# Optimization experiments

Measured on AMD Instinct MI355X. Metric: run time of the kernel, lower is better.

The kernel has to match this reference:

```python
import jax, jax.numpy as jnp
import numpy as np

EPS_DIST = 1e-8   # matches 1.0/(dist + 1e-08) in the torch module
NEG_SLOPE = 0.2   # deep_gcns act_layer leakyrelu default
BN_EPS = 1e-5


def setup_inputs() -> dict:
    key = jax.random.key(0)
    ks = jax.random.split(key, 6)
    B, N, M = 8, 2048, 8192
    C, C_skip = 512, 256
    C_in = C + C_skip          # 768
    H1, H2 = 512, 256          # up_conv_nn = [768, 512, 256]
    pos = jax.random.normal(ks[0], (B, N, 3), dtype=jnp.float32)
    pos_skip = jax.random.normal(ks[1], (B, M, 3), dtype=jnp.float32)
    x = jax.random.normal(ks[2], (B, C, N), dtype=jnp.float32)
    x_skip = jax.random.normal(ks[3], (B, C_skip, M), dtype=jnp.float32)
    W1 = jax.random.normal(ks[4], (H1, C_in), dtype=jnp.float32) * (1.0 / np.sqrt(C_in))
    W2 = jax.random.normal(ks[5], (H2, H1), dtype=jnp.float32) * (1.0 / np.sqrt(H1))
    return {
        "pos": pos, "pos_skip": pos_skip, "x": x, "x_skip": x_skip,
        "W1": W1, "gamma1": jnp.ones((H1,), jnp.float32), "beta1": jnp.zeros((H1,), jnp.float32),
        "W2": W2, "gamma2": jnp.ones((H2,), jnp.float32), "beta2": jnp.zeros((H2,), jnp.float32),
    }


def _three_nn(query, ref):
    # query: [B, M, 3], ref: [B, N, 3] -> dist [B, M, 3], idx [B, M, 3]
    q2 = jnp.sum(query * query, axis=-1)                 # [B, M]
    r2 = jnp.sum(ref * ref, axis=-1)                     # [B, N]
    d2 = q2[:, :, None] + r2[:, None, :] - 2.0 * jnp.einsum('bmd,bnd->bmn', query, ref)
    neg_d2, idx = jax.lax.top_k(-d2, 3)                  # 3 smallest squared dists
    dist = jnp.sqrt(jnp.maximum(-neg_d2, 0.0))           # tp.three_nn returns L2 distance
    return dist, idx


def _three_interpolate(x, idx, weight):
    # x: [B, C, N], idx: [B, M, 3], weight: [B, M, 3] -> [B, C, M]
    xT = jnp.transpose(x, (0, 2, 1))                     # [B, N, C]
    gathered = jax.vmap(lambda f, i: f[i])(xT, idx)      # [B, M, 3, C]
    return jnp.einsum('bmkc,bmk->bcm', gathered, weight)


def _bn_act(h, gamma, beta):
    # training-mode BatchNorm1d over (batch, points) + LeakyReLU
    mean = jnp.mean(h, axis=(0, 2), keepdims=True)
    var = jnp.mean((h - mean) ** 2, axis=(0, 2), keepdims=True)
    h = (h - mean) * jax.lax.rsqrt(var + BN_EPS)
    h = h * gamma[None, :, None] + beta[None, :, None]
    return jnp.where(h >= 0, h, NEG_SLOPE * h)


def reference(pos, pos_skip, x, x_skip, W1, gamma1, beta1, W2, gamma2, beta2):
    # 3-NN of each fine point (pos_skip) among coarse points (pos)
    dist, idx = _three_nn(pos_skip, pos)
    dist_recip = 1.0 / (dist + EPS_DIST)
    norm = jnp.sum(dist_recip, axis=2, keepdims=True)
    weight = dist_recip / norm                           # [B, M, 3]
    interpolated = _three_interpolate(x, idx, weight)    # [B, C, M]
    feats = jnp.concatenate([interpolated, x_skip], axis=1)  # [B, C+C_skip, M]
    # MLP: Conv1d(k=1, bias=False) -> BN -> LeakyReLU, twice
    h = jnp.einsum('oi,bim->bom', W1, feats)
    h = _bn_act(h, gamma1, beta1)
    h = jnp.einsum('oi,bim->bom', W2, h)
    h = _bn_act(h, gamma2, beta2)
    return h  # [B, 256, M]
```

## Files before the change

### kernel.cpp

```cpp
#include <hip/hip_runtime.h>
#include <stdint.h>

#define B_    8
#define N_    2048
#define M_    8192
#define C_    512
#define CSK   256
#define CIN   768
#define H1C   512
#define H2C   256
#define NCOL  65536
typedef unsigned short u16;
typedef __attribute__((ext_vector_type(8))) short  s16x8;
typedef __attribute__((ext_vector_type(4))) float  f32x4;

__device__ inline u16 f2bf(float f) {
    unsigned u = __float_as_uint(f);
    unsigned r = (u + 0x7fffu + ((u >> 16) & 1u)) >> 16;
    return (u16)r;
}
__device__ inline float bflo(unsigned u) { return __uint_as_float(u << 16); }
__device__ inline float bfhi(unsigned u) { return __uint_as_float(u & 0xffff0000u); }

__global__ __launch_bounds__(256) void cvt_bf16_k(const float* __restrict__ in,
                                                  u16* __restrict__ out, int n4) {
    const int i = blockIdx.x * 256 + threadIdx.x;
    if (i >= n4) return;
    const float4 v = *(const float4*)(in + (size_t)i * 4);
    u16 o[4] = {f2bf(v.x), f2bf(v.y), f2bf(v.z), f2bf(v.w)};
    *(uint2*)(out + (size_t)i * 4) = *(uint2*)o;
}

__device__ inline void ins3(float d, int n,
                            float& d0, int& i0, float& d1, int& i1,
                            float& d2, int& i2) {
    const bool lt0 = d < d0, lt1 = d < d1, lt2 = d < d2;
    const float nd2 = lt1 ? d1 : (lt2 ? d : d2);
    const int   ni2 = lt1 ? i1 : (lt2 ? n : i2);
    const float nd1 = lt0 ? d0 : (lt1 ? d : d1);
    const int   ni1 = lt0 ? i0 : (lt1 ? n : i1);
    const float nd0 = lt0 ? d : d0;
    const int   ni0 = lt0 ? n : i0;
    d0 = nd0; d1 = nd1; d2 = nd2; i0 = ni0; i1 = ni1; i2 = ni2;
}

__global__ __launch_bounds__(256) void knn_kernel(const float* __restrict__ pos,
                                                  const float* __restrict__ pos_skip,
                                                  int* __restrict__ idx_out,
                                                  float* __restrict__ w_out) {
    __shared__ float rpx[N_], rpy[N_], rpz[N_], rr2[N_];
    const int b = blockIdx.y;
    const int tid = threadIdx.x;
    for (int t = tid; t < N_ * 3; t += 256) {
        const float v = pos[(size_t)b * N_ * 3 + t];
        const int n = t / 3, k = t - n * 3;
        if (k == 0) rpx[n] = v; else if (k == 1) rpy[n] = v; else rpz[n] = v;
    }
    __syncthreads();
    for (int n = tid; n < N_; n += 256)
        rr2[n] = rpx[n] * rpx[n] + rpy[n] * rpy[n] + rpz[n] * rpz[n];
    __syncthreads();

    const int q = tid >> 3;
    const int part = tid & 7;
    const int m = blockIdx.x * 32 + q;
    const size_t qoff = ((size_t)b * M_ + m) * 3;
    const float qx = pos_skip[qoff], qy = pos_skip[qoff + 1], qz = pos_skip[qoff + 2];
    const float q2x = -2.0f * qx, q2y = -2.0f * qy, q2z = -2.0f * qz;
    const float qq = qx * qx + qy * qy + qz * qz;

    float d0 = 1e30f, d1 = 1e30f, d2 = 1e30f;
    int i0 = 0, i1 = 0, i2 = 0;
#pragma unroll 4
    for (int i = 0; i < 64; ++i) {
        const int n = part * 4 + i * 32;
        const float4 xx = *(const float4*)&rpx[n];
        const float4 yy = *(const float4*)&rpy[n];
        const float4 zz = *(const float4*)&rpz[n];
        const float4 ww = *(const float4*)&rr2[n];
        const float s0 = fmaf(xx.x, q2x, fmaf(yy.x, q2y, fmaf(zz.x, q2z, ww.x)));
        const float s1 = fmaf(xx.y, q2x, fmaf(yy.y, q2y, fmaf(zz.y, q2z, ww.y)));
        const float s2 = fmaf(xx.z, q2x, fmaf(yy.z, q2y, fmaf(zz.z, q2z, ww.z)));
        const float s3 = fmaf(xx.w, q2x, fmaf(yy.w, q2y, fmaf(zz.w, q2z, ww.w)));
        ins3(s0, n + 0, d0, i0, d1, i1, d2, i2);
        ins3(s1, n + 1, d0, i0, d1, i1, d2, i2);
        ins3(s2, n + 2, d0, i0, d1, i1, d2, i2);
        ins3(s3, n + 3, d0, i0, d1, i1, d2, i2);
    }

#pragma unroll
    for (int xm = 1; xm <= 4; xm <<= 1) {
        const float od0 = __shfl_xor(d0, xm), od1 = __shfl_xor(d1, xm), od2 = __shfl_xor(d2, xm);
        const int   oi0 = __shfl_xor(i0, xm), oi1 = __shfl_xor(i1, xm), oi2 = __shfl_xor(i2, xm);
        ins3(od0, oi0, d0, i0, d1, i1, d2, i2);
        ins3(od1, oi1, d0, i0, d1, i1, d2, i2);
        ins3(od2, oi2, d0, i0, d1, i1, d2, i2);
    }

    if (part == 0) {
        const float dd0 = fmaxf(d0 + qq, 0.f);
        const float dd1 = fmaxf(d1 + qq, 0.f);
        const float dd2 = fmaxf(d2 + qq, 0.f);
        const float r0 = 1.0f / (sqrtf(dd0) + 1e-8f);
        const float r1 = 1.0f / (sqrtf(dd1) + 1e-8f);
        const float r2 = 1.0f / (sqrtf(dd2) + 1e-8f);
        const float inv = 1.0f / (r0 + r1 + r2);
        const size_t o = ((size_t)b * M_ + m) * 3;
        idx_out[o] = i0; idx_out[o + 1] = i1; idx_out[o + 2] = i2;
        w_out[o] = r0 * inv; w_out[o + 1] = r1 * inv; w_out[o + 2] = r2 * inv;
    }
}

__global__ __launch_bounds__(256) void transpose_x(const float* __restrict__ x,
                                                   u16* __restrict__ xT) {
    __shared__ float t[32][33];
    const int tx = threadIdx.x & 31, ty = threadIdx.x >> 5;
    const int n0 = blockIdx.x * 32, c0 = blockIdx.y * 32, b = blockIdx.z;
#pragma unroll
    for (int r = 0; r < 4; ++r) {
        const int c = c0 + ty + r * 8;
        t[ty + r * 8][tx] = x[((size_t)b * C_ + c) * N_ + n0 + tx];
    }
    __syncthreads();
#pragma unroll
    for (int r = 0; r < 4; ++r) {
        const int n = n0 + ty + r * 8;
        xT[((size_t)b * N_ + n) * C_ + c0 + tx] = f2bf(t[tx][ty + r * 8]);
    }
}

__global__ __launch_bounds__(256) void feats_skip(const float* __restrict__ xs,
                                                  u16* __restrict__ Fsk) {
    __shared__ float t[32][33];
    const int tx = threadIdx.x & 31, ty = threadIdx.x >> 5;
    const int m0 = blockIdx.x * 32, c0 = blockIdx.y * 32, b = blockIdx.z;
#pragma unroll
    for (int r = 0; r < 4; ++r) {
        const int c = c0 + ty + r * 8;
        t[ty + r * 8][tx] = xs[((size_t)b * CSK + c) * M_ + m0 + tx];
    }
    __syncthreads();
#pragma unroll
    for (int r = 0; r < 4; ++r) {
        const int m = m0 + ty + r * 8;
        Fsk[((size_t)b * M_ + m) * CSK + c0 + tx] = f2bf(t[tx][ty + r * 8]);
    }
}

__device__ inline unsigned interp_pk(unsigned a, unsigned b, unsigned c,
                                     float w0, float w1, float w2) {
    const float lo = w0 * bflo(a) + w1 * bflo(b) + w2 * bflo(c);
    const float hi = w0 * bfhi(a) + w1 * bfhi(b) + w2 * bfhi(c);
    return (unsigned)f2bf(lo) | ((unsigned)f2bf(hi) << 16);
}

__device__ inline void stage64(u16* lds, const char* gbase, int ld2,
                               int lane, int wv) {
    const int slot = (lane & 7) ^ (lane >> 3);
#pragma unroll
    for (int jj = 0; jj < 4; ++jj) {
        const int chunk = jj * 4 + wv;
        const int row = chunk * 8 + (lane >> 3);
        const char* g = gbase + (size_t)row * ld2 + slot * 16;
        __builtin_amdgcn_global_load_lds(
            (const __attribute__((address_space(1))) void*)g,
            (__attribute__((address_space(3))) void*)((char*)lds + chunk * 1024),
            16, 0, 0);
    }
}

__global__ __launch_bounds__(256) void gemm1(const u16* __restrict__ W1b,
                                             const u16* __restrict__ xT,
                                             const u16* __restrict__ Fsk,
                                             const int* __restrict__ idx,
                                             const float* __restrict__ w,
                                             u16* __restrict__ H1,
                                             float* __restrict__ ps1,
                                             float* __restrict__ pq1) {
    __shared__ __attribute__((aligned(16))) u16 As[128 * 64];
    __shared__ __attribute__((aligned(16))) u16 Bs[128 * 64];
    __shared__ float lsum[2][128], lsq[2][128];
    __shared__ int   sIdx[128][3];
    __shared__ float sW[128][3];
    const int tid = threadIdx.x;
    const int lane = tid & 63, wv = tid >> 6;
    const int wr = wv >> 1, wc = wv & 1;
    const int l15 = lane & 15, l4 = lane >> 4;
    const int v = (blockIdx.x & 7) * 256 + (blockIdx.x >> 3);
    const int rowblk = v & 3, colblk = v >> 2;
    const int rowM0 = rowblk * 128, colN0 = colblk * 128;
    const int b = colN0 >> 13;
    f32x4 acc[4][4] = {};
    const char* Ab = (const char*)(W1b + (size_t)rowM0 * CIN);
    const u16* xTb = xT + (size_t)b * N_ * C_;

    for (int t = tid; t < 384; t += 256) {
        const int rr = t / 3, kk = t - rr * 3;
        const size_t gi = ((size_t)colN0 + rr) * 3 + kk;
        sIdx[rr][kk] = idx[gi];
        sW[rr][kk]   = w[gi];
    }
    __syncthreads();

    const int prow = tid >> 3;
    const int slot = tid & 7;
    const int kk_off = slot * 8;

    for (int kt = 0; kt < CIN / 64; ++kt) {
        stage64(As, Ab + kt * 128, CIN * 2, lane, wv);
        uint4 bp[4];
        if (kt < 8) {
            const int kk = kt * 64 + kk_off;
#pragma unroll
            for (int p = 0; p < 4; ++p) {
                const int row = p * 32 + prow;
                const uint4 a = *(const uint4*)(xTb + (size_t)sIdx[row][0] * C_ + kk);
                const uint4 c = *(const uint4*)(xTb + (size_t)sIdx[row][1] * C_ + kk);
                const uint4 d = *(const uint4*)(xTb + (size_t)sIdx[row][2] * C_ + kk);
                const float w0 = sW[row][0], w1 = sW[row][1], w2 = sW[row][2];
                bp[p].x = interp_pk(a.x, c.x, d.x, w0, w1, w2);
                bp[p].y = interp_pk(a.y, c.y, d.y, w0, w1, w2);
                bp[p].z = interp_pk(a.z, c.z, d.z, w0, w1, w2);
                bp[p].w = interp_pk(a.w, c.w, d.w, w0, w1, w2);
            }
        } else {
            const int kk = (kt - 8) * 64 + kk_off;
#pragma unroll
            for (int p = 0; p < 4; ++p) {
                const int row = p * 32 + prow;
                bp[p] = *(const uint4*)(Fsk + (size_t)(colN0 + row) * CSK + kk);
            }
        }
#pragma unroll
        for (int p = 0; p < 4; ++p) {
            const int row = p * 32 + prow;
            const int s = slot ^ (row & 7);
            *(uint4*)((char*)Bs + row * 128 + s * 16) = bp[p];
        }
        __syncthreads();
#pragma unroll
        for (int ks = 0; ks < 2; ++ks) {
            s16x8 af[4], bfr[4];
#pragma unroll
            for (int i = 0; i < 4; ++i) {
                const int R = wr * 64 + i * 16 + l15;
                const int s = ((ks << 2) | l4) ^ (R & 7);
                af[i] = *(const s16x8*)((const char*)As + R * 128 + s * 16);
            }
#pragma unroll
            for (int j = 0; j < 4; ++j) {
                const int R = wc * 64 + j * 16 + l15;
                const int s = ((ks << 2) | l4) ^ (R & 7);
                bfr[j] = *(const s16x8*)((const char*)Bs + R * 128 + s * 16);
            }
#pragma unroll
            for (int i = 0; i < 4; ++i)
#pragma unroll
                for (int j = 0; j < 4; ++j)
                    acc[i][j] = __builtin_amdgcn_mfma_f32_16x16x32_bf16(bfr[j], af[i], acc[i][j], 0, 0, 0);
        }
        __syncthreads();
    }

#pragma unroll
    for (int i = 0; i < 4; ++i) {
        const int o = rowM0 + wr * 64 + i * 16 + l15;
#pragma unroll
        for (int j = 0; j < 4; ++j) {
            const int colb = colN0 + wc * 64 + j * 16 + l4 * 4;
#pragma unroll
            for (int r = 0; r < 4; ++r)
                H1[(size_t)(colb + r) * H1C + o] = f2bf(acc[i][j][r]);
        }
    }

#pragma unroll
    for (int i = 0; i < 4; ++i) {
        float s = 0.f, q = 0.f;
#pragma unroll
        for (int j = 0; j < 4; ++j)
#pragma unroll
            for (int r = 0; r < 4; ++r) {
                const float vv = acc[i][j][r];
                s += vv; q += vv * vv;
            }
        s += __shfl_xor(s, 16); q += __shfl_xor(q, 16);
        s += __shfl_xor(s, 32); q += __shfl_xor(q, 32);
        if ((lane & 48) == 0) {
            lsum[wc][wr * 64 + i * 16 + l15] = s;
            lsq [wc][wr * 64 + i * 16 + l15] = q;
        }
    }
    __syncthreads();
    if (tid < 128) {
        const float S = lsum[0][tid] + lsum[1][tid];
        const float Q = lsq[0][tid] + lsq[1][tid];
        ps1[(size_t)(rowM0 + tid) * 512 + colblk] = S;
        pq1[(size_t)(rowM0 + tid) * 512 + colblk] = Q;
    }
}

__global__ __launch_bounds__(256) void bn1_final(const float* __restrict__ ps,
                                                 const float* __restrict__ pq,
                                                 const float* __restrict__ gamma,
                                                 const float* __restrict__ beta,
                                                 float* __restrict__ sc,
                                                 float* __restrict__ sh) {
    const int o = blockIdx.x;
    const int t = threadIdx.x;
    float S = ps[(size_t)o * 512 + t] + ps[(size_t)o * 512 + 256 + t];
    float Q = pq[(size_t)o * 512 + t] + pq[(size_t)o * 512 + 256 + t];
    __shared__ float rs[256], rq[256];
    rs[t] = S; rq[t] = Q;
    __syncthreads();
    for (int st = 128; st > 0; st >>= 1) {
        if (t < st) { rs[t] += rs[t + st]; rq[t] += rq[t + st]; }
        __syncthreads();
    }
    if (t == 0) {
        const float mean = rs[0] * (1.0f / NCOL);
        const float var  = fmaxf(rq[0] * (1.0f / NCOL) - mean * mean, 0.f);
        const float is   = rsqrtf(var + 1e-5f);
        const float s    = gamma[o] * is;
        sc[o] = s;
        sh[o] = beta[o] - mean * s;
    }
}

__device__ inline void stage2A(u16* dst, const u16* W2b, int k0,
                               int lane, int wv) {
#pragma unroll
    for (int h = 0; h < 2; ++h) {
        const int p_loc = h * 128 + wv * 16 + (lane >> 2);
        const u16* g = W2b + (size_t)p_loc * H1C + k0 + (lane & 3) * 8;
        __builtin_amdgcn_global_load_lds(
            (const __attribute__((address_space(1))) void*)g,
            (__attribute__((address_space(3))) void*)((char*)dst + (h * 512 + wv * 64) * 16),
            16, 0, 0);
    }
}

__global__ __launch_bounds__(512, 2) void gemm2(const u16* __restrict__ W2b,
                                                const u16* __restrict__ H1,
                                                const float* __restrict__ sc1,
                                                const float* __restrict__ sh1,
                                                float* __restrict__ out,
                                                float* __restrict__ ps2,
                                                float* __restrict__ pq2) {
    __shared__ __attribute__((aligned(16))) u16 As[2][256 * 32];
    __shared__ __attribute__((aligned(16))) u16 Bs[2][256 * 32];
    __shared__ float lsum[4][256], lsq[4][256];
    __shared__ float scs[512], shs[512];
    const int tid = threadIdx.x;
    const int lane = tid & 63, wv = tid >> 6;
    const int pgrp = wv & 1, cgrp = wv >> 1;
    const int l15 = lane & 15, l4 = lane >> 4;
    const int col0 = blockIdx.x * 256;
    const u16* Hb = H1 + (size_t)col0 * H1C;
    const int kb = (lane & 3) * 8;
    const int prow0 = wv * 16 + (lane >> 2);
    f32x4 acc[4][8] = {};

    scs[tid] = sc1[tid];
    shs[tid] = sh1[tid];

    stage2A(As[0], W2b, 0, lane, wv);
    uint4 nb0 = *(const uint4*)(Hb + (size_t)prow0 * H1C + kb);
    uint4 nb1 = *(const uint4*)(Hb + (size_t)(prow0 + 128) * H1C + kb);
    __syncthreads();

    auto xformB = [&](int buf, uint4 b0, uint4 b1, int k0) {
        const f32x4 s0v = *(const f32x4*)&scs[k0 + kb];
        const f32x4 s1v = *(const f32x4*)&scs[k0 + kb + 4];
        const f32x4 h0v = *(const f32x4*)&shs[k0 + kb];
        const f32x4 h1v = *(const f32x4*)&shs[k0 + kb + 4];
        const float sv[8] = {s0v[0], s0v[1], s0v[2], s0v[3], s1v[0], s1v[1], s1v[2], s1v[3]};
        const float hv[8] = {h0v[0], h0v[1], h0v[2], h0v[3], h1v[0], h1v[1], h1v[2], h1v[3]};
        uint4 bw[2] = {b0, b1};
#pragma unroll
        for (int h = 0; h < 2; ++h) {
            unsigned uu[4] = {bw[h].x, bw[h].y, bw[h].z, bw[h].w};
            unsigned rr[4];
#pragma unroll
            for (int e = 0; e < 4; ++e) {
                float f0 = fmaf(bflo(uu[e]), sv[e * 2], hv[e * 2]);
                float f1 = fmaf(bfhi(uu[e]), sv[e * 2 + 1], hv[e * 2 + 1]);
                f0 = f0 >= 0.f ? f0 : 0.2f * f0;
                f1 = f1 >= 0.f ? f1 : 0.2f * f1;
                rr[e] = (unsigned)f2bf(f0) | ((unsigned)f2bf(f1) << 16);
            }
            *(uint4*)&Bs[buf][(size_t)(h * 512 + wv * 64 + lane) * 8] = make_uint4(rr[0], rr[1], rr[2], rr[3]);
        }
    };

    xformB(0, nb0, nb1, 0);
    __syncthreads();

    int cur = 0;
    for (int step = 0; step < 16; ++step) {
        if (step < 15) {
            const int k0 = (step + 1) * 32;
            stage2A(As[cur ^ 1], W2b, k0, lane, wv);
            nb0 = *(const uint4*)(Hb + (size_t)prow0 * H1C + k0 + kb);
            nb1 = *(const uint4*)(Hb + (size_t)(prow0 + 128) * H1C + k0 + kb);
        }
        const u16* Ac = As[cur];
        const u16* Bc = Bs[cur];
        s16x8 af[8], bfr[4];
#pragma unroll
        for (int pf = 0; pf < 8; ++pf)
            af[pf] = *(const s16x8*)&Ac[(pgrp * 128 + pf * 16 + l15) * 32 + l4 * 8];
#pragma unroll
        for (int cf = 0; cf < 4; ++cf)
            bfr[cf] = *(const s16x8*)&Bc[(cgrp * 64 + cf * 16 + l15) * 32 + l4 * 8];
#pragma unroll
        for (int cf = 0; cf < 4; ++cf)
#pragma unroll
            for (int pf = 0; pf < 8; ++pf)
                acc[cf][pf] = __builtin_amdgcn_mfma_f32_16x16x32_bf16(bfr[cf], af[pf], acc[cf][pf], 0, 0, 0);
        if (step < 15) {
            xformB(cur ^ 1, nb0, nb1, (step + 1) * 32);
        }
        __syncthreads();
        cur ^= 1;
    }

    const int bidx = col0 >> 13;
    const int mb   = col0 & (M_ - 1);
#pragma unroll
    for (int cf = 0; cf < 4; ++cf) {
#pragma unroll
        for (int pf = 0; pf < 8; ++pf) {
            const int p  = pgrp * 128 + pf * 16 + l15;
            const int mm = mb + cgrp * 64 + cf * 16 + l4 * 4;
            *(f32x4*)(out + (size_t)bidx * (H2C * M_) + (size_t)p * M_ + mm) = acc[cf][pf];
        }
    }

#pragma unroll
    for (int pf = 0; pf < 8; ++pf) {
        float s = 0.f, q = 0.f;
#pragma unroll
        for (int cf = 0; cf < 4; ++cf)
#pragma unroll
            for (int r = 0; r < 4; ++r) {
                const float vv = acc[cf][pf][r];
                s += vv; q += vv * vv;
            }
        s += __shfl_xor(s, 16); q += __shfl_xor(q, 16);
        s += __shfl_xor(s, 32); q += __shfl_xor(q, 32);
        if ((lane & 48) == 0) {
            lsum[cgrp][pgrp * 128 + pf * 16 + l15] = s;
            lsq [cgrp][pgrp * 128 + pf * 16 + l15] = q;
        }
    }
    __syncthreads();
    if (tid < 256) {
        const float S = lsum[0][tid] + lsum[1][tid] + lsum[2][tid] + lsum[3][tid];
        const float Q = lsq[0][tid] + lsq[1][tid] + lsq[2][tid] + lsq[3][tid];
        ps2[(size_t)tid * 256 + blockIdx.x] = S;
        pq2[(size_t)tid * 256 + blockIdx.x] = Q;
    }
}

__global__ __launch_bounds__(256) void bn2_final(const float* __restrict__ ps,
                                                 const float* __restrict__ pq,
                                                 const float* __restrict__ gamma,
                                                 const float* __restrict__ beta,
                                                 float* __restrict__ sc,
                                                 float* __restrict__ sh) {
    const int p = blockIdx.x;
    const int t = threadIdx.x;
    float S = ps[(size_t)p * 256 + t];
    float Q = pq[(size_t)p * 256 + t];
    __shared__ float rs[256], rq[256];
    rs[t] = S; rq[t] = Q;
    __syncthreads();
    for (int st = 128; st > 0; st >>= 1) {
        if (t < st) { rs[t] += rs[t + st]; rq[t] += rq[t + st]; }
        __syncthreads();
    }
    if (t == 0) {
        const float mean = rs[0] * (1.0f / NCOL);
        const float var  = fmaxf(rq[0] * (1.0f / NCOL) - mean * mean, 0.f);
        const float is   = rsqrtf(var + 1e-5f);
        const float s    = gamma[p] * is;
        sc[p] = s;
        sh[p] = beta[p] - mean * s;
    }
}

__global__ __launch_bounds__(256) void bn_apply2(float* __restrict__ out,
                                                 const float* __restrict__ sc,
                                                 const float* __restrict__ sh) {
    const size_t i = (size_t)blockIdx.x * 256 + threadIdx.x;
    const int p = (int)((i >> 13) & (H2C - 1));
    float v = out[i];
    v = fmaf(v, sc[p], sh[p]);
    out[i] = v >= 0.f ? v : 0.2f * v;
}

extern "C" void kernel_launch(void* const* d_in, const int* in_sizes, int n_in,
                              void* d_out, int out_size, void* d_ws, size_t ws_size,
                              hipStream_t stream) {
    const float* pos      = (const float*)d_in[0];
    const float* pos_skip = (const float*)d_in[1];
    const float* x        = (const float*)d_in[2];
    const float* x_skip   = (const float*)d_in[3];
    const float* W1       = (const float*)d_in[4];
    const float* gamma1   = (const float*)d_in[5];
    const float* beta1    = (const float*)d_in[6];
    const float* W2       = (const float*)d_in[7];
    const float* gamma2   = (const float*)d_in[8];
    const float* beta2    = (const float*)d_in[9];
    float* out = (float*)d_out;

    char* ws = (char*)d_ws;
    size_t off = 0;
    auto alloc = [&](size_t bytes) {
        void* p = ws + off;
        off = (off + bytes + 255) & ~(size_t)255;
        return p;
    };
    int*   idx   = (int*)  alloc((size_t)NCOL * 3 * sizeof(int));
    float* w     = (float*)alloc((size_t)NCOL * 3 * sizeof(float));
    u16*   xT    = (u16*)  alloc((size_t)B_ * N_ * C_ * sizeof(u16));
    u16*   W1b   = (u16*)  alloc((size_t)H1C * CIN * sizeof(u16));
    u16*   W2b   = (u16*)  alloc((size_t)H2C * H1C * sizeof(u16));
    u16*   Fsk   = (u16*)  alloc((size_t)NCOL * CSK * sizeof(u16));
    u16*   H1    = (u16*)  alloc((size_t)NCOL * H1C * sizeof(u16));
    float* ps1   = (float*)alloc((size_t)H1C * 512 * sizeof(float));
    float* pq1   = (float*)alloc((size_t)H1C * 512 * sizeof(float));
    float* ps2   = (float*)alloc((size_t)H2C * 256 * sizeof(float));
    float* pq2   = (float*)alloc((size_t)H2C * 256 * sizeof(float));
    float* sc1   = (float*)alloc(H1C * sizeof(float));
    float* sh1   = (float*)alloc(H1C * sizeof(float));
    float* sc2   = (float*)alloc(H2C * sizeof(float));
    float* sh2   = (float*)alloc(H2C * sizeof(float));

    cvt_bf16_k<<<(H1C * CIN / 4 + 255) / 256, 256, 0, stream>>>(W1, W1b, H1C * CIN / 4);
    cvt_bf16_k<<<(H2C * H1C / 4 + 255) / 256, 256, 0, stream>>>(W2, W2b, H2C * H1C / 4);
    knn_kernel<<<dim3(M_ / 32, B_), 256, 0, stream>>>(pos, pos_skip, idx, w);
    transpose_x<<<dim3(N_ / 32, C_ / 32, B_), 256, 0, stream>>>(x, xT);
    feats_skip<<<dim3(M_ / 32, CSK / 32, B_), 256, 0, stream>>>(x_skip, Fsk);
    gemm1<<<2048, 256, 0, stream>>>(W1b, xT, Fsk, idx, w, H1, ps1, pq1);
    bn1_final<<<H1C, 256, 0, stream>>>(ps1, pq1, gamma1, beta1, sc1, sh1);
    gemm2<<<NCOL / 256, 512, 0, stream>>>(W2b, H1, sc1, sh1, out, ps2, pq2);
    bn2_final<<<H2C, 256, 0, stream>>>(ps2, pq2, gamma2, beta2, sc2, sh2);
    bn_apply2<<<(int)(((size_t)NCOL * H2C) / 256), 256, 0, stream>>>(out, sc2, sh2);
}
```

Before: 293.3 us.

## Double-buffer gemm1 LDS tiles to overlap gathers with MFMA compute

Splits the A and B shared-memory tiles into two buffers and restructures the K loop. The next tile's W1 slice and the interpolation gathers are issued before the current tile's MFMAs, and the interpolated result is written into the alternate buffer afterward. This hides global-load and gather latency behind matrix math and removes one barrier per iteration. In exchange it doubles LDS use for the tiles, which may lower occupancy, and keeps twelve uint4 registers live across the MFMA loop.

```diff
diff --git a/kernel.cpp b/kernel.cpp
--- a/kernel.cpp
+++ b/kernel.cpp
@@ -177,8 +177,8 @@
                                              u16* __restrict__ H1,
                                              float* __restrict__ ps1,
                                              float* __restrict__ pq1) {
-    __shared__ __attribute__((aligned(16))) u16 As[128 * 64];
-    __shared__ __attribute__((aligned(16))) u16 Bs[128 * 64];
+    __shared__ __attribute__((aligned(16))) u16 As[2][128 * 64];
+    __shared__ __attribute__((aligned(16))) u16 Bs[2][128 * 64];
     __shared__ float lsum[2][128], lsq[2][128];
     __shared__ int   sIdx[128][3];
     __shared__ float sW[128][3];
@@ -206,38 +206,59 @@
     const int slot = tid & 7;
     const int kk_off = slot * 8;
 
-    for (int kt = 0; kt < CIN / 64; ++kt) {
-        stage64(As, Ab + kt * 128, CIN * 2, lane, wv);
-        uint4 bp[4];
+    uint4 gA[4], gC[4], gD[4];
+
+    auto gatherB = [&](int kt) {
         if (kt < 8) {
             const int kk = kt * 64 + kk_off;
 #pragma unroll
             for (int p = 0; p < 4; ++p) {
                 const int row = p * 32 + prow;
-                const uint4 a = *(const uint4*)(xTb + (size_t)sIdx[row][0] * C_ + kk);
-                const uint4 c = *(const uint4*)(xTb + (size_t)sIdx[row][1] * C_ + kk);
-                const uint4 d = *(const uint4*)(xTb + (size_t)sIdx[row][2] * C_ + kk);
-                const float w0 = sW[row][0], w1 = sW[row][1], w2 = sW[row][2];
-                bp[p].x = interp_pk(a.x, c.x, d.x, w0, w1, w2);
-                bp[p].y = interp_pk(a.y, c.y, d.y, w0, w1, w2);
-                bp[p].z = interp_pk(a.z, c.z, d.z, w0, w1, w2);
-                bp[p].w = interp_pk(a.w, c.w, d.w, w0, w1, w2);
+                gA[p] = *(const uint4*)(xTb + (size_t)sIdx[row][0] * C_ + kk);
+                gC[p] = *(const uint4*)(xTb + (size_t)sIdx[row][1] * C_ + kk);
+                gD[p] = *(const uint4*)(xTb + (size_t)sIdx[row][2] * C_ + kk);
             }
         } else {
             const int kk = (kt - 8) * 64 + kk_off;
 #pragma unroll
             for (int p = 0; p < 4; ++p) {
                 const int row = p * 32 + prow;
-                bp[p] = *(const uint4*)(Fsk + (size_t)(colN0 + row) * CSK + kk);
-            }
-        }
+                gA[p] = *(const uint4*)(Fsk + (size_t)(colN0 + row) * CSK + kk);
+            }
+        }
+    };
+    auto writeB = [&](int kt, int buf) {
 #pragma unroll
         for (int p = 0; p < 4; ++p) {
             const int row = p * 32 + prow;
             const int s = slot ^ (row & 7);
-            *(uint4*)((char*)Bs + row * 128 + s * 16) = bp[p];
-        }
-        __syncthreads();
+            uint4 bp;
+            if (kt < 8) {
+                const float w0 = sW[row][0], w1 = sW[row][1], w2 = sW[row][2];
+                bp.x = interp_pk(gA[p].x, gC[p].x, gD[p].x, w0, w1, w2);
+                bp.y = interp_pk(gA[p].y, gC[p].y, gD[p].y, w0, w1, w2);
+                bp.z = interp_pk(gA[p].z, gC[p].z, gD[p].z, w0, w1, w2);
+                bp.w = interp_pk(gA[p].w, gC[p].w, gD[p].w, w0, w1, w2);
+            } else {
+                bp = gA[p];
+            }
+            *(uint4*)((char*)Bs[buf] + row * 128 + s * 16) = bp;
+        }
+    };
+
+    stage64(As[0], Ab + 0, CIN * 2, lane, wv);
+    gatherB(0);
+    writeB(0, 0);
+    __syncthreads();
+
+    int cur = 0;
+    for (int kt = 0; kt < CIN / 64; ++kt) {
+        if (kt < CIN / 64 - 1) {
+            stage64(As[cur ^ 1], Ab + (kt + 1) * 128, CIN * 2, lane, wv);
+            gatherB(kt + 1);
+        }
+        const u16* Ac = As[cur];
+        const u16* Bc = Bs[cur];
 #pragma unroll
         for (int ks = 0; ks < 2; ++ks) {
             s16x8 af[4], bfr[4];
@@ -245,13 +266,13 @@
             for (int i = 0; i < 4; ++i) {
                 const int R = wr * 64 + i * 16 + l15;
                 const int s = ((ks << 2) | l4) ^ (R & 7);
-                af[i] = *(const s16x8*)((const char*)As + R * 128 + s * 16);
+                af[i] = *(const s16x8*)((const char*)Ac + R * 128 + s * 16);
             }
 #pragma unroll
             for (int j = 0; j < 4; ++j) {
                 const int R = wc * 64 + j * 16 + l15;
                 const int s = ((ks << 2) | l4) ^ (R & 7);
-                bfr[j] = *(const s16x8*)((const char*)Bs + R * 128 + s * 16);
+                bfr[j] = *(const s16x8*)((const char*)Bc + R * 128 + s * 16);
             }
 #pragma unroll
             for (int i = 0; i < 4; ++i)
@@ -259,7 +280,9 @@
                 for (int j = 0; j < 4; ++j)
                     acc[i][j] = __builtin_amdgcn_mfma_f32_16x16x32_bf16(bfr[j], af[i], acc[i][j], 0, 0, 0);
         }
+        if (kt < CIN / 64 - 1) writeB(kt + 1, cur ^ 1);
         __syncthreads();
+        cur ^= 1;
     }
 
 #pragma unroll
```

Measured after the change: 409.7 us. +39.7%, slower.
